# Performance work log

Measured on AMD Instinct MI355X. Metric: run time of the kernel, lower is better.

## Reference

```python
import jax, jax.numpy as jnp
import numpy as np


def setup_inputs() -> dict:
    key = jax.random.key(0)
    x = jax.random.normal(key, (64, 128, 1024), dtype=jnp.float32)
    return {"x": x}


def reference(x):
    # x: (batch, dim, feature)
    b, d, T = x.shape
    X = jnp.fft.rfft(x, axis=2)[:, :, 1:-1]          # (b, d, K) drop DC & Nyquist, K = T//2 - 1
    f = jnp.fft.rfftfreq(T)[1:-1].astype(x.dtype)    # (K,)
    t = jnp.arange(T, dtype=x.dtype)                 # (T,)
    ang = (2.0 * jnp.pi) * f[:, None] * t[None, :]   # (K, T) shared basis angles
    # Original sums amp*cos(2*pi*f*t + phase) over the +f and -f (conjugate)
    # copies; the two terms are identical, giving 2*amp*cos(2*pi*f*t + phase).
    # Expand via cos(a+p) = cos(a)cos(p) - sin(a)sin(p) with
    # amp*cos(phase) = Re(X), amp*sin(phase) = Im(X)  ->  two GEMMs over K.
    re = jnp.real(X)                                  # (b, d, K)
    im = jnp.imag(X)                                  # (b, d, K)
    out = 2.0 * (jnp.einsum('bdk,kt->bdt', re, jnp.cos(ang))
                 - jnp.einsum('bdk,kt->bdt', im, jnp.sin(ang)))
    return out                                        # (b, d, T)
```

## Files before the change

### kernel.cpp

```cpp
#include <hip/hip_runtime.h>


#define T_LEN 1024
#define ROWS (64 * 128)

typedef float vf4 __attribute__((ext_vector_type(4)));

__global__ __launch_bounds__(256) void season_block_46428596469890_kernel(
    const float* __restrict__ x, float* __restrict__ out) {
    const int row  = blockIdx.x * 4 + (threadIdx.x >> 6);
    const int lane = threadIdx.x & 63;

    const vf4* xrow = (const vf4*)(x + (size_t)row * T_LEN);
    vf4* orow       = (vf4*)(out + (size_t)row * T_LEN);

    vf4 v[4];
    #pragma unroll
    for (int i = 0; i < 4; ++i) v[i] = xrow[lane + 64 * i];

    float s0 = 0.0f, sN = 0.0f;
    #pragma unroll
    for (int i = 0; i < 4; ++i) {
        s0 += (v[i].x + v[i].y) + (v[i].z + v[i].w);
        sN += (v[i].x - v[i].y) + (v[i].z - v[i].w);
    }

    #pragma unroll
    for (int off = 1; off < 64; off <<= 1) {
        s0 += __shfl_xor(s0, off, 64);
        sN += __shfl_xor(sN, off, 64);
    }

    #pragma unroll
    for (int i = 0; i < 4; ++i) {
        vf4 o;
        o.x = 1024.0f * v[i].x - s0 - sN;
        o.y = 1024.0f * v[i].y - s0 + sN;
        o.z = 1024.0f * v[i].z - s0 - sN;
        o.w = 1024.0f * v[i].w - s0 + sN;
        __builtin_nontemporal_store(o, &orow[lane + 64 * i]);
    }
}

extern "C" void kernel_launch(void* const* d_in, const int* in_sizes, int n_in,
                              void* d_out, int out_size, void* d_ws, size_t ws_size,
                              hipStream_t stream) {
    const float* x = (const float*)d_in[0];
    float* out = (float*)d_out;
    season_block_46428596469890_kernel<<<ROWS / 4, 256, 0, stream>>>(x, out);
}
```

Measured before the change: 79.51 us.

## Process four rows per wave with software-prefetched next-row loads

Each wavefront now handles four consecutive rows instead of one, loading the next row into registers while reducing and writing the current one. The grid shrinks by four, so fewer waves are launched and per-wave setup is amortised. The output expression is also folded into fused multiply-adds with precomputed offsets. The risk is fewer waves in flight to hide memory latency on a bandwidth-bound copy-like kernel, plus higher register use.

```diff
diff --git a/kernel.cpp b/kernel.cpp
--- a/kernel.cpp
+++ b/kernel.cpp
@@ -3,42 +3,58 @@
 
 #define T_LEN 1024
 #define ROWS (64 * 128)
+#define ROWS_PER_WAVE 4
 
 typedef float vf4 __attribute__((ext_vector_type(4)));
 
 __global__ __launch_bounds__(256) void season_block_46428596469890_kernel(
     const float* __restrict__ x, float* __restrict__ out) {
-    const int row  = blockIdx.x * 4 + (threadIdx.x >> 6);
+    const int wave = blockIdx.x * 4 + (threadIdx.x >> 6);
     const int lane = threadIdx.x & 63;
 
-    const vf4* xrow = (const vf4*)(x + (size_t)row * T_LEN);
-    vf4* orow       = (vf4*)(out + (size_t)row * T_LEN);
+    const size_t base = (size_t)wave * ROWS_PER_WAVE * T_LEN;
+    const vf4* xr = (const vf4*)(x + base);
+    vf4* orow     = (vf4*)(out + base);
 
-    vf4 v[4];
+    vf4 a[4], b[4];
     #pragma unroll
-    for (int i = 0; i < 4; ++i) v[i] = xrow[lane + 64 * i];
-
-    float s0 = 0.0f, sN = 0.0f;
-    #pragma unroll
-    for (int i = 0; i < 4; ++i) {
-        s0 += (v[i].x + v[i].y) + (v[i].z + v[i].w);
-        sN += (v[i].x - v[i].y) + (v[i].z - v[i].w);
-    }
+    for (int i = 0; i < 4; ++i) a[i] = xr[lane + 64 * i];
 
     #pragma unroll
-    for (int off = 1; off < 64; off <<= 1) {
-        s0 += __shfl_xor(s0, off, 64);
-        sN += __shfl_xor(sN, off, 64);
-    }
+    for (int k = 0; k < ROWS_PER_WAVE; ++k) {
+        if (k < ROWS_PER_WAVE - 1) {
+            #pragma unroll
+            for (int i = 0; i < 4; ++i)
+                b[i] = xr[(k + 1) * (T_LEN / 4) + lane + 64 * i];
+        }
 
-    #pragma unroll
-    for (int i = 0; i < 4; ++i) {
-        vf4 o;
-        o.x = 1024.0f * v[i].x - s0 - sN;
-        o.y = 1024.0f * v[i].y - s0 + sN;
-        o.z = 1024.0f * v[i].z - s0 - sN;
-        o.w = 1024.0f * v[i].w - s0 + sN;
-        __builtin_nontemporal_store(o, &orow[lane + 64 * i]);
+        float s0 = 0.0f, sN = 0.0f;
+        #pragma unroll
+        for (int i = 0; i < 4; ++i) {
+            s0 += (a[i].x + a[i].y) + (a[i].z + a[i].w);
+            sN += (a[i].x - a[i].y) + (a[i].z - a[i].w);
+        }
+
+        #pragma unroll
+        for (int off = 1; off < 64; off <<= 1) {
+            s0 += __shfl_xor(s0, off, 64);
+            sN += __shfl_xor(sN, off, 64);
+        }
+
+        const float ea = s0 + sN;
+        const float eb = s0 - sN;
+        #pragma unroll
+        for (int i = 0; i < 4; ++i) {
+            vf4 o;
+            o.x = __builtin_fmaf(1024.0f, a[i].x, -ea);
+            o.y = __builtin_fmaf(1024.0f, a[i].y, -eb);
+            o.z = __builtin_fmaf(1024.0f, a[i].z, -ea);
+            o.w = __builtin_fmaf(1024.0f, a[i].w, -eb);
+            __builtin_nontemporal_store(o, &orow[k * (T_LEN / 4) + lane + 64 * i]);
+        }
+
+        #pragma unroll
+        for (int i = 0; i < 4; ++i) a[i] = b[i];
     }
 }
 
@@ -47,5 +63,5 @@
                               hipStream_t stream) {
     const float* x = (const float*)d_in[0];
     float* out = (float*)d_out;
-    season_block_46428596469890_kernel<<<ROWS / 4, 256, 0, stream>>>(x, out);
+    season_block_46428596469890_kernel<<<ROWS / ROWS_PER_WAVE / 4, 256, 0, stream>>>(x, out);
 }
```

Result: no change. 80.14 us (+0.8%).
